# Kernel tuning notes

Measured on AMD Instinct MI355X. Metric: run time of the kernel, lower is better.

## Reference

```python
import jax, jax.numpy as jnp
import numpy as np

EPS = 1e-13

def masked_softmax(scores, mask):
    # scores: (B, L1, L2), mask: (B, L2) float {0,1}
    m = mask[:, None, :]
    # faithful to ESIM masked_softmax: softmax(scores * mask), re-mask, renormalize
    p = jax.nn.softmax(scores * m, axis=-1) * m
    return p / (jnp.sum(p, axis=-1, keepdims=True) + EPS)

def weighted_sum(values, weights, mask):
    # values: (B, Lv, H), weights: (B, Lq, Lv), mask: (B, Lq)
    out = jnp.einsum('bqv,bvh->bqh', weights, values)
    return out * mask[:, :, None]

def setup_inputs() -> dict:
    key = jax.random.key(0)
    k1, k2, k3, k4 = jax.random.split(key, 4)
    B, P, Q, H = 64, 1024, 1024, 256
    pre_batch = jax.random.normal(k1, (B, P, H), dtype=jnp.float32)
    hypo_batch = jax.random.normal(k2, (B, Q, H), dtype=jnp.float32)
    pre_mask = jax.random.randint(k3, (B, P), 0, 2, dtype=jnp.int32).at[:, 0].set(1)
    hypo_mask = jax.random.randint(k4, (B, Q), 0, 2, dtype=jnp.int32).at[:, 0].set(1)
    return {"pre_batch": pre_batch, "pre_mask": pre_mask,
            "hypo_batch": hypo_batch, "hypo_mask": hypo_mask}

def reference(pre_batch, pre_mask, hypo_batch, hypo_mask):
    pre_m = pre_mask.astype(pre_batch.dtype)
    hypo_m = hypo_mask.astype(hypo_batch.dtype)
    # similarity: (B, P, Q)
    similarity = jnp.einsum('bph,bqh->bpq', pre_batch, hypo_batch)
    pre_hypo_attn = masked_softmax(similarity, hypo_m)                       # (B,P,Q)
    hypo_pre_attn = masked_softmax(jnp.swapaxes(similarity, 1, 2), pre_m)    # (B,Q,P)
    attented_pre = weighted_sum(hypo_batch, pre_hypo_attn, pre_m)            # (B,P,H)
    attented_hypo = weighted_sum(pre_batch, hypo_pre_attn, hypo_m)           # (B,Q,H)
    return (attented_pre, attented_hypo)
```

## Files before the change

kernel.cpp:

```cpp
#include <hip/hip_runtime.h>
#include <stdint.h>

#define NB 64
#define NN 1024
#define NH 256

typedef _Float16 h8v __attribute__((ext_vector_type(8)));
typedef float    f4v __attribute__((ext_vector_type(4)));
typedef uint32_t u4v __attribute__((ext_vector_type(4)));
typedef uint32_t u2v __attribute__((ext_vector_type(2)));

static __device__ __forceinline__ uint32_t pack2h(float a, float b) {
  uint32_t ua = (uint32_t)__builtin_bit_cast(uint16_t, (_Float16)a);
  uint32_t ub = (uint32_t)__builtin_bit_cast(uint16_t, (_Float16)b);
  return ua | (ub << 16);
}

static __device__ __forceinline__ void gl_lds16(const void* g, void* l) {
  __builtin_amdgcn_global_load_lds(
      (const __attribute__((address_space(1))) uint32_t*)g,
      (__attribute__((address_space(3))) uint32_t*)l, 16, 0, 0);
}

__global__ __launch_bounds__(256)
void prep_tiles(const float* __restrict__ pre, const float* __restrict__ hypo,
                uint8_t* __restrict__ img)
{
  const int id = blockIdx.x;
  const int m  = id >> 11;
  const int bt = id & 2047;
  const float* src = (m ? hypo : pre) + (size_t)bt * (32 * NH);
  uint8_t* kimg = img + (size_t)id * 32768;
  uint8_t* vimg = kimg + 16384;

  __shared__ __align__(16) float ft[32 * 260];
  const int t = threadIdx.x, w = t >> 6, lane = t & 63;

#pragma unroll
  for (int i = 0; i < 8; ++i) {
    const int row = w * 8 + i;
    gl_lds16(src + row * NH + lane * 4, (uint8_t*)ft + row * 1040);
  }
  __syncthreads();

#pragma unroll
  for (int c = 0; c < 4; ++c) {
    const int k = c * 8 + (t >> 5);
    const uint32_t X = (uint32_t)((t & 31) * 16);
    const uint32_t h0 = ((X >> 4) ^ (uint32_t)(k & 7)) * 8;
    const uint8_t* p = (const uint8_t*)ft + k * 1040 + h0 * 4;
    f4v a0 = *(const f4v*)p;
    f4v a1 = *(const f4v*)(p + 16);
    u4v o; o[0] = pack2h(a0[0], a0[1]); o[1] = pack2h(a0[2], a0[3]);
    o[2] = pack2h(a1[0], a1[1]); o[3] = pack2h(a1[2], a1[3]);
    *(u4v*)(kimg + c * 4096 + t * 16) = o;
  }
  {
    const int g2 = t >> 6;
#pragma unroll
    for (int c = 0; c < 4; ++c) {
      const int h = c * 64 + (t & 63);
      float v[8];
#pragma unroll
      for (int j = 0; j < 4; ++j) v[j]     = ft[(4 * g2 + j) * 260 + h];
#pragma unroll
      for (int j = 0; j < 4; ++j) v[4 + j] = ft[(16 + 4 * g2 + j) * 260 + h];
      u4v o; o[0] = pack2h(v[0], v[1]); o[1] = pack2h(v[2], v[3]);
      o[2] = pack2h(v[4], v[5]); o[3] = pack2h(v[6], v[7]);
      *(u4v*)(vimg + g2 * 4096 + h * 16) = o;
    }
  }
}

__global__ __launch_bounds__(256, 2)
void attn_img(const uint8_t* __restrict__ img,
              const int* __restrict__ pre_mask, const int* __restrict__ hypo_mask,
              float* __restrict__ out)
{
  const int fid  = blockIdx.x;
  const int xcd  = fid & 7;
  const int s    = fid >> 3;
  const int bp   = xcd * 16 + (s >> 3);
  const int rblk = s & 7;
  const int pass = bp >> 6;
  const int b    = bp & 63;

  const uint8_t* qimg  = img + (size_t)(pass ? 1 : 0) * 67108864;
  const uint8_t* kvimg = img + (size_t)(pass ? 0 : 1) * 67108864;
  const int* kmask = pass == 0 ? hypo_mask : pre_mask;
  const int* qmask = pass == 0 ? pre_mask  : hypo_mask;
  float* outp = out + ((size_t)pass * NB + b) * NN * NH;
  const uint8_t* kvb = kvimg + (size_t)b * (32 * 32768);
  const int* kmb = kmask + b * NN;

  __shared__ __align__(16) uint8_t sbuf[2][32768];
  __shared__ __align__(16) float sbias[NN];

  const int t    = threadIdx.x;
  const int lane = t & 63;
  const int w    = t >> 6;
  const int g    = lane >> 4;
  const int q    = lane & 15;

  for (int i = t; i < NN; i += 256) sbias[i] = kmb[i] ? 0.f : -1e30f;

  h8v qf0[8], qf1[8];
  {
    const uint8_t* qb = qimg + (size_t)b * (32 * 32768);
#pragma unroll
    for (int ff = 0; ff < 2; ++ff) {
      const int qrow = rblk * 128 + w * 32 + ff * 16 + q;
      const uint8_t* qt = qb + (size_t)(qrow >> 5) * 32768 + (qrow & 31) * 512;
      const uint32_t swq = (uint32_t)((qrow & 7) << 4);
#pragma unroll
      for (int c = 0; c < 8; ++c) {
        h8v v = *(const h8v*)(qt + (((uint32_t)((c * 4 + g) << 4)) ^ swq));
        if (ff == 0) qf0[c] = v; else qf1[c] = v;
      }
    }
  }

  f4v accA[16], accB[16];
#pragma unroll
  for (int cf = 0; cf < 16; ++cf) { accA[cf] = (f4v){0,0,0,0}; accB[cf] = (f4v){0,0,0,0}; }
  float mrunA = -1e30f, lrunA = 0.f, mrunB = -1e30f, lrunB = 0.f;

#pragma unroll
  for (int i = 0; i < 8; ++i)
    gl_lds16(kvb + w * 8192 + i * 1024 + lane * 16, &sbuf[0][0] + w * 8192 + i * 1024);
  __syncthreads();

#pragma unroll 1
  for (int kt = 0; kt < 32; ++kt) {
    const int cur = kt & 1;
    if (kt < 31) {
      const uint8_t* kvt = kvb + (size_t)(kt + 1) * 32768;
#pragma unroll
      for (int i = 0; i < 8; ++i)
        gl_lds16(kvt + w * 8192 + i * 1024 + lane * 16,
                 &sbuf[cur ^ 1][0] + w * 8192 + i * 1024);
    }
    const uint8_t* sK = &sbuf[cur][0];
    const uint8_t* sV = sK + 16384;
    const int kb = kt * 32;

    const f4v b0 = *(const f4v*)&sbias[kb + 4 * g];
    const f4v b1 = *(const f4v*)&sbias[kb + 16 + 4 * g];

    f4v s0A = (f4v){0,0,0,0}, s1A = (f4v){0,0,0,0};
    f4v s0B = (f4v){0,0,0,0}, s1B = (f4v){0,0,0,0};
    __builtin_amdgcn_s_setprio(1);
#pragma unroll
    for (int c = 0; c < 8; ++c) {
      const uint32_t a0 = (uint32_t)(q * 512) + (((uint32_t)(c * 64 + g * 16)) ^ ((uint32_t)((q & 7) << 4)));
      h8v k0 = *(const h8v*)(sK + a0);
      h8v k1 = *(const h8v*)(sK + a0 + 8192);
      s0A = __builtin_amdgcn_mfma_f32_16x16x32_f16(k0, qf0[c], s0A, 0, 0, 0);
      s0B = __builtin_amdgcn_mfma_f32_16x16x32_f16(k0, qf1[c], s0B, 0, 0, 0);
      s1A = __builtin_amdgcn_mfma_f32_16x16x32_f16(k1, qf0[c], s1A, 0, 0, 0);
      s1B = __builtin_amdgcn_mfma_f32_16x16x32_f16(k1, qf1[c], s1B, 0, 0, 0);
    }
    __builtin_amdgcn_s_setprio(0);

    f4v sb0A, sb1A, sb0B, sb1B;
#pragma unroll
    for (int r = 0; r < 4; ++r) {
      sb0A[r] = s0A[r] + b0[r];  sb1A[r] = s1A[r] + b1[r];
      sb0B[r] = s0B[r] + b0[r];  sb1B[r] = s1B[r] + b1[r];
    }
    float tA = fmaxf(sb0A[0], sb1A[0]), tB = fmaxf(sb0B[0], sb1B[0]);
#pragma unroll
    for (int r = 1; r < 4; ++r) {
      tA = fmaxf(tA, fmaxf(sb0A[r], sb1A[r]));
      tB = fmaxf(tB, fmaxf(sb0B[r], sb1B[r]));
    }
    tA = fmaxf(tA, __shfl_xor(tA, 16));  tB = fmaxf(tB, __shfl_xor(tB, 16));
    tA = fmaxf(tA, __shfl_xor(tA, 32));  tB = fmaxf(tB, __shfl_xor(tB, 32));

    const bool grow = __any(fmaxf(tA - mrunA, tB - mrunB) > 8.0f);
    if (grow) {
      const float mnA = fmaxf(mrunA, tA), mnB = fmaxf(mrunB, tB);
      const float sA = __expf(mrunA - mnA), sB = __expf(mrunB - mnB);
      mrunA = mnA; mrunB = mnB;
      lrunA *= sA; lrunB *= sB;
#pragma unroll
      for (int cf = 0; cf < 16; ++cf) {
#pragma unroll
        for (int r = 0; r < 4; ++r) {
          accA[cf][r] *= sA;
          accB[cf][r] *= sB;
        }
      }
    }

    float pA[8], pB[8];
    float psA = 0.f, psB = 0.f;
#pragma unroll
    for (int r = 0; r < 4; ++r) {
      float a0 = __expf(sb0A[r] - mrunA);
      float a1 = __expf(sb1A[r] - mrunA);
      float b0e = __expf(sb0B[r] - mrunB);
      float b1e = __expf(sb1B[r] - mrunB);
      pA[r] = a0; pA[4 + r] = a1; psA += a0 + a1;
      pB[r] = b0e; pB[4 + r] = b1e; psB += b0e + b1e;
    }
    psA += __shfl_xor(psA, 16);  psB += __shfl_xor(psB, 16);
    psA += __shfl_xor(psA, 32);  psB += __shfl_xor(psB, 32);
    lrunA += psA; lrunB += psB;

    u4v au, bu;
    au[0] = pack2h(pA[0], pA[1]); au[1] = pack2h(pA[2], pA[3]);
    au[2] = pack2h(pA[4], pA[5]); au[3] = pack2h(pA[6], pA[7]);
    bu[0] = pack2h(pB[0], pB[1]); bu[1] = pack2h(pB[2], pB[3]);
    bu[2] = pack2h(pB[4], pB[5]); bu[3] = pack2h(pB[6], pB[7]);
    const h8v apA = __builtin_bit_cast(h8v, au);
    const h8v apB = __builtin_bit_cast(h8v, bu);

    __builtin_amdgcn_s_setprio(1);
#pragma unroll
    for (int cf = 0; cf < 16; ++cf) {
      h8v av = *(const h8v*)(sV + (uint32_t)(g * 4096 + (cf * 16 + q) * 16));
      accA[cf] = __builtin_amdgcn_mfma_f32_16x16x32_f16(av, apA, accA[cf], 0, 0, 0);
      accB[cf] = __builtin_amdgcn_mfma_f32_16x16x32_f16(av, apB, accB[cf], 0, 0, 0);
    }
    __builtin_amdgcn_s_setprio(0);

    __syncthreads();
  }

#pragma unroll
  for (int ff = 0; ff < 2; ++ff) {
    const float lrun = ff ? lrunB : lrunA;
    const int qrow = rblk * 128 + w * 32 + ff * 16 + q;
    const float fac = (float)qmask[b * NN + qrow] / lrun;
    float* op = outp + (size_t)qrow * NH;
#pragma unroll
    for (int cf = 0; cf < 16; ++cf) {
      f4v v = ff ? accB[cf] : accA[cf];
      v[0] *= fac; v[1] *= fac; v[2] *= fac; v[3] *= fac;
      *(f4v*)(op + cf * 16 + 4 * g) = v;
    }
  }
}

__global__ __launch_bounds__(256, 2)
void fused_dual_attn_fb(const float* __restrict__ pre,  const int* __restrict__ pre_mask,
                        const float* __restrict__ hypo, const int* __restrict__ hypo_mask,
                        float* __restrict__ out)
{
  const int pass = blockIdx.z;
  const float* Qm  = pass == 0 ? pre  : hypo;
  const float* KVm = pass == 0 ? hypo : pre;
  const int* kmask = pass == 0 ? hypo_mask : pre_mask;
  const int* qmask = pass == 0 ? pre_mask  : hypo_mask;
  float* outp = out + (size_t)pass * NB * NN * NH;

  const int b  = blockIdx.y;
  const int r0 = blockIdx.x * 64;

  __shared__ __align__(16) unsigned char sK [32 * NH * 2];
  __shared__ __align__(16) unsigned char sVt[NH * 16 * 4];
  __shared__ int smask[NN];

  const int t    = threadIdx.x;
  const int lane = t & 63;
  const int w    = t >> 6;
  const int g    = lane >> 4;
  const int q    = lane & 15;

  for (int i = t; i < NN; i += 256) smask[i] = kmask[b * NN + i];

  const int qrow = r0 + w * 16 + q;
  h8v qf[8];
  {
    const float* qp = Qm + ((size_t)b * NN + qrow) * NH + g * 8;
#pragma unroll
    for (int c = 0; c < 8; ++c) {
      f4v a0 = *(const f4v*)(qp + c * 32);
      f4v a1 = *(const f4v*)(qp + c * 32 + 4);
      h8v v;
      v[0] = (_Float16)a0[0]; v[1] = (_Float16)a0[1];
      v[2] = (_Float16)a0[2]; v[3] = (_Float16)a0[3];
      v[4] = (_Float16)a1[0]; v[5] = (_Float16)a1[1];
      v[6] = (_Float16)a1[2]; v[7] = (_Float16)a1[3];
      qf[c] = v;
    }
  }

  f4v acc[16];
#pragma unroll
  for (int cf = 0; cf < 16; ++cf) acc[cf] = (f4v){0.f, 0.f, 0.f, 0.f};
  float mrun = -1e30f, lrun = 0.f;

  const int skey = t & 31;
  const int m16  = (t >> 1) & 15;
  const int scb  = (t >> 5) << 2;
  const int odd  = skey & 1;

  for (int kb = 0; kb < NN; kb += 32) {
    __syncthreads();
#pragma unroll
    for (int i = 0; i < 8; ++i) {
      const int col = scb + 32 * i;
      f4v v = *(const f4v*)(KVm + ((size_t)b * NN + kb + skey) * NH + col);
      u2v d; d[0] = pack2h(v[0], v[1]); d[1] = pack2h(v[2], v[3]);
      uint32_t ka = (uint32_t)(skey * 512 + col * 2) ^ (uint32_t)((skey & 7) << 4);
      *(u2v*)(sK + ka) = d;
      float e = odd ? v[0] : v[2];
      float f = odd ? v[1] : v[3];
      float oe = __shfl_xor(e, 1);
      float of = __shfl_xor(f, 1);
      float lo0 = odd ? oe   : v[0];
      float hi0 = odd ? v[2] : oe;
      float lo1 = odd ? of   : v[1];
      float hi1 = odd ? v[3] : of;
      const int h0 = col + odd * 2;
      *(uint32_t*)(sVt + (uint32_t)((h0    ) * 64 + m16 * 4)) = pack2h(lo0, hi0);
      *(uint32_t*)(sVt + (uint32_t)((h0 + 1) * 64 + m16 * 4)) = pack2h(lo1, hi1);
    }
    __syncthreads();

    f4v s0 = (f4v){0.f,0.f,0.f,0.f}, s1 = (f4v){0.f,0.f,0.f,0.f};
#pragma unroll
    for (int c = 0; c < 8; ++c) {
      uint32_t a0 = ((uint32_t)(q * 512 + c * 64 + g * 16)) ^ (uint32_t)((q & 7) << 4);
      uint32_t a1 = ((uint32_t)((16 + q) * 512 + c * 64 + g * 16)) ^ (uint32_t)((q & 7) << 4);
      h8v k0 = *(const h8v*)(sK + a0);
      h8v k1 = *(const h8v*)(sK + a1);
      s0 = __builtin_amdgcn_mfma_f32_16x16x32_f16(k0, qf[c], s0, 0, 0, 0);
      s1 = __builtin_amdgcn_mfma_f32_16x16x32_f16(k1, qf[c], s1, 0, 0, 0);
    }

    int msk[8];
#pragma unroll
    for (int r = 0; r < 4; ++r) {
      msk[r]     = smask[kb + 4 * g + r];
      msk[4 + r] = smask[kb + 16 + 4 * g + r];
    }
    float tmax = -1e30f;
#pragma unroll
    for (int r = 0; r < 4; ++r)
      tmax = fmaxf(tmax, fmaxf(msk[r] ? s0[r] : -1e30f, msk[4 + r] ? s1[r] : -1e30f));
    tmax = fmaxf(tmax, __shfl_xor(tmax, 16));
    tmax = fmaxf(tmax, __shfl_xor(tmax, 32));
    const float mnew = fmaxf(mrun, tmax);
    const float scl = __expf(mrun - mnew);
    mrun = mnew;

    float p[8];
    float psum = 0.f;
#pragma unroll
    for (int r = 0; r < 4; ++r) {
      float p0 = msk[r]     ? __expf(s0[r] - mnew) : 0.f;
      float p1 = msk[4 + r] ? __expf(s1[r] - mnew) : 0.f;
      p[r] = p0; p[4 + r] = p1;
      psum += p0 + p1;
    }
    psum += __shfl_xor(psum, 16);
    psum += __shfl_xor(psum, 32);
    lrun = lrun * scl + psum;

    float srow[4];
#pragma unroll
    for (int r = 0; r < 4; ++r) srow[r] = __shfl(scl, 4 * g + r);
#pragma unroll
    for (int cf = 0; cf < 16; ++cf) {
#pragma unroll
      for (int r = 0; r < 4; ++r) acc[cf][r] *= srow[r];
    }

    uint32_t pf00 = pack2h(p[0], p[1]);
    uint32_t pf01 = pack2h(p[2], p[3]);
    uint32_t pf10 = pack2h(p[4], p[5]);
    uint32_t pf11 = pack2h(p[6], p[7]);
    const int srcA = q + 16 * ((2 * g) & 3);
    const int srcB = srcA + 16;
    uint32_t w0a = __shfl(pf00, srcA), w1a = __shfl(pf01, srcA);
    uint32_t w0b = __shfl(pf00, srcB), w1b = __shfl(pf01, srcB);
    uint32_t x0a = __shfl(pf10, srcA), x1a = __shfl(pf11, srcA);
    uint32_t x0b = __shfl(pf10, srcB), x1b = __shfl(pf11, srcB);
    u4v au;
    au[0] = (g >= 2) ? x0a : w0a;
    au[1] = (g >= 2) ? x1a : w1a;
    au[2] = (g >= 2) ? x0b : w0b;
    au[3] = (g >= 2) ? x1b : w1b;
    const h8v ap = __builtin_bit_cast(h8v, au);

#pragma unroll
    for (int cf = 0; cf < 16; ++cf) {
      h8v bv = *(const h8v*)(sVt + (uint32_t)((cf * 16 + q) * 64 + g * 16));
      acc[cf] = __builtin_amdgcn_mfma_f32_16x16x32_f16(ap, bv, acc[cf], 0, 0, 0);
    }
  }

  float fac[4];
#pragma unroll
  for (int r = 0; r < 4; ++r) {
    const float lr = __shfl(lrun, 4 * g + r);
    const int row = r0 + w * 16 + 4 * g + r;
    fac[r] = (float)qmask[b * NN + row] / lr;
  }
  float* op = outp + ((size_t)b * NN + r0 + w * 16) * NH;
#pragma unroll
  for (int cf = 0; cf < 16; ++cf) {
#pragma unroll
    for (int r = 0; r < 4; ++r) {
      op[(4 * g + r) * NH + cf * 16 + q] = acc[cf][r] * fac[r];
    }
  }
}

extern "C" void kernel_launch(void* const* d_in, const int* in_sizes, int n_in,
                              void* d_out, int out_size, void* d_ws, size_t ws_size,
                              hipStream_t stream) {
  const float* pre       = (const float*)d_in[0];
  const int*   pre_mask  = (const int*)d_in[1];
  const float* hypo      = (const float*)d_in[2];
  const int*   hypo_mask = (const int*)d_in[3];
  float* out = (float*)d_out;
  (void)in_sizes; (void)n_in; (void)out_size;

  if (ws_size >= (size_t)2 * 67108864) {
    uint8_t* img = (uint8_t*)d_ws;
    prep_tiles<<<dim3(4096), dim3(256), 0, stream>>>(pre, hypo, img);
    attn_img<<<dim3(1024), dim3(256), 0, stream>>>(img, pre_mask, hypo_mask, out);
  } else {
    fused_dual_attn_fb<<<dim3(16, 64, 2), dim3(256), 0, stream>>>(pre, pre_mask, hypo, hypo_mask, out);
  }
}
```

Measured before the change: 222.2 us.

## Halve query rows per block, single-buffer KV tile, raise occupancy to three blocks

Each wave now handles 16 query rows instead of 32, so each block covers 64 rows and the grid doubles to 2048 blocks. The KV shared buffer drops from double to single buffering, with a sync before and after each tile load. Launch bounds now ask for three blocks per CU. The goal is to cut registers and LDS per block so more waves are resident and hide latency. In exchange each K/V tile is reused by half as many query rows, which doubles total KV traffic, and the loss of prefetch exposes load latency unless other resident blocks cover it.

```diff
diff --git a/kernel.cpp b/kernel.cpp
--- a/kernel.cpp
+++ b/kernel.cpp
@@ -72,7 +72,7 @@
   }
 }
 
-__global__ __launch_bounds__(256, 2)
+__global__ __launch_bounds__(256, 3)
 void attn_img(const uint8_t* __restrict__ img,
               const int* __restrict__ pre_mask, const int* __restrict__ hypo_mask,
               float* __restrict__ out)
@@ -80,8 +80,8 @@
   const int fid  = blockIdx.x;
   const int xcd  = fid & 7;
   const int s    = fid >> 3;
-  const int bp   = xcd * 16 + (s >> 3);
-  const int rblk = s & 7;
+  const int bp   = xcd * 16 + (s >> 4);
+  const int rblk = s & 15;
   const int pass = bp >> 6;
   const int b    = bp & 63;
 
@@ -93,7 +93,7 @@
   const uint8_t* kvb = kvimg + (size_t)b * (32 * 32768);
   const int* kmb = kmask + b * NN;
 
-  __shared__ __align__(16) uint8_t sbuf[2][32768];
+  __shared__ __align__(16) uint8_t sbuf[32768];
   __shared__ __align__(16) float sbias[NN];
 
   const int t    = threadIdx.x;
@@ -104,139 +104,108 @@
 
   for (int i = t; i < NN; i += 256) sbias[i] = kmb[i] ? 0.f : -1e30f;
 
-  h8v qf0[8], qf1[8];
+  h8v qf[8];
   {
     const uint8_t* qb = qimg + (size_t)b * (32 * 32768);
-#pragma unroll
-    for (int ff = 0; ff < 2; ++ff) {
-      const int qrow = rblk * 128 + w * 32 + ff * 16 + q;
-      const uint8_t* qt = qb + (size_t)(qrow >> 5) * 32768 + (qrow & 31) * 512;
-      const uint32_t swq = (uint32_t)((qrow & 7) << 4);
-#pragma unroll
-      for (int c = 0; c < 8; ++c) {
-        h8v v = *(const h8v*)(qt + (((uint32_t)((c * 4 + g) << 4)) ^ swq));
-        if (ff == 0) qf0[c] = v; else qf1[c] = v;
-      }
-    }
-  }
-
-  f4v accA[16], accB[16];
-#pragma unroll
-  for (int cf = 0; cf < 16; ++cf) { accA[cf] = (f4v){0,0,0,0}; accB[cf] = (f4v){0,0,0,0}; }
-  float mrunA = -1e30f, lrunA = 0.f, mrunB = -1e30f, lrunB = 0.f;
-
-#pragma unroll
-  for (int i = 0; i < 8; ++i)
-    gl_lds16(kvb + w * 8192 + i * 1024 + lane * 16, &sbuf[0][0] + w * 8192 + i * 1024);
-  __syncthreads();
+    const int qrow = rblk * 64 + w * 16 + q;
+    const uint8_t* qt = qb + (size_t)(qrow >> 5) * 32768 + (qrow & 31) * 512;
+    const uint32_t swq = (uint32_t)((qrow & 7) << 4);
+#pragma unroll
+    for (int c = 0; c < 8; ++c)
+      qf[c] = *(const h8v*)(qt + (((uint32_t)((c * 4 + g) << 4)) ^ swq));
+  }
+
+  f4v acc[16];
+#pragma unroll
+  for (int cf = 0; cf < 16; ++cf) acc[cf] = (f4v){0, 0, 0, 0};
+  float mrun = -1e30f, lrun = 0.f;
 
 #pragma unroll 1
   for (int kt = 0; kt < 32; ++kt) {
-    const int cur = kt & 1;
-    if (kt < 31) {
-      const uint8_t* kvt = kvb + (size_t)(kt + 1) * 32768;
+    __syncthreads();
+    {
+      const uint8_t* ktile = kvb + (size_t)kt * 32768;
 #pragma unroll
       for (int i = 0; i < 8; ++i)
-        gl_lds16(kvt + w * 8192 + i * 1024 + lane * 16,
-                 &sbuf[cur ^ 1][0] + w * 8192 + i * 1024);
-    }
-    const uint8_t* sK = &sbuf[cur][0];
+        gl_lds16(ktile + w * 8192 + i * 1024 + lane * 16,
+                 &sbuf[0] + w * 8192 + i * 1024);
+    }
+    __syncthreads();
+
+    const uint8_t* sK = &sbuf[0];
     const uint8_t* sV = sK + 16384;
     const int kb = kt * 32;
 
     const f4v b0 = *(const f4v*)&sbias[kb + 4 * g];
     const f4v b1 = *(const f4v*)&sbias[kb + 16 + 4 * g];
 
-    f4v s0A = (f4v){0,0,0,0}, s1A = (f4v){0,0,0,0};
-    f4v s0B = (f4v){0,0,0,0}, s1B = (f4v){0,0,0,0};
+    f4v s0 = (f4v){0, 0, 0, 0}, s1 = (f4v){0, 0, 0, 0};
     __builtin_amdgcn_s_setprio(1);
 #pragma unroll
     for (int c = 0; c < 8; ++c) {
       const uint32_t a0 = (uint32_t)(q * 512) + (((uint32_t)(c * 64 + g * 16)) ^ ((uint32_t)((q & 7) << 4)));
       h8v k0 = *(const h8v*)(sK + a0);
       h8v k1 = *(const h8v*)(sK + a0 + 8192);
-      s0A = __builtin_amdgcn_mfma_f32_16x16x32_f16(k0, qf0[c], s0A, 0, 0, 0);
-      s0B = __builtin_amdgcn_mfma_f32_16x16x32_f16(k0, qf1[c], s0B, 0, 0, 0);
-      s1A = __builtin_amdgcn_mfma_f32_16x16x32_f16(k1, qf0[c], s1A, 0, 0, 0);
-      s1B = __builtin_amdgcn_mfma_f32_16x16x32_f16(k1, qf1[c], s1B, 0, 0, 0);
+      s0 = __builtin_amdgcn_mfma_f32_16x16x32_f16(k0, qf[c], s0, 0, 0, 0);
+      s1 = __builtin_amdgcn_mfma_f32_16x16x32_f16(k1, qf[c], s1, 0, 0, 0);
     }
     __builtin_amdgcn_s_setprio(0);
 
-    f4v sb0A, sb1A, sb0B, sb1B;
+    f4v sb0, sb1;
+#pragma unroll
+    for (int r = 0; r < 4; ++r) { sb0[r] = s0[r] + b0[r]; sb1[r] = s1[r] + b1[r]; }
+    float tmax = fmaxf(sb0[0], sb1[0]);
+#pragma unroll
+    for (int r = 1; r < 4; ++r) tmax = fmaxf(tmax, fmaxf(sb0[r], sb1[r]));
+    tmax = fmaxf(tmax, __shfl_xor(tmax, 16));
+    tmax = fmaxf(tmax, __shfl_xor(tmax, 32));
+
+    const bool grow = __any(tmax - mrun > 8.0f);
+    if (grow) {
+      const float mn = fmaxf(mrun, tmax);
+      const float sc = __expf(mrun - mn);
+      mrun = mn; lrun *= sc;
+#pragma unroll
+      for (int cf = 0; cf < 16; ++cf) {
+#pragma unroll
+        for (int r = 0; r < 4; ++r) acc[cf][r] *= sc;
+      }
+    }
+
+    float p[8];
+    float psum = 0.f;
 #pragma unroll
     for (int r = 0; r < 4; ++r) {
-      sb0A[r] = s0A[r] + b0[r];  sb1A[r] = s1A[r] + b1[r];
-      sb0B[r] = s0B[r] + b0[r];  sb1B[r] = s1B[r] + b1[r];
-    }
-    float tA = fmaxf(sb0A[0], sb1A[0]), tB = fmaxf(sb0B[0], sb1B[0]);
-#pragma unroll
-    for (int r = 1; r < 4; ++r) {
-      tA = fmaxf(tA, fmaxf(sb0A[r], sb1A[r]));
-      tB = fmaxf(tB, fmaxf(sb0B[r], sb1B[r]));
-    }
-    tA = fmaxf(tA, __shfl_xor(tA, 16));  tB = fmaxf(tB, __shfl_xor(tB, 16));
-    tA = fmaxf(tA, __shfl_xor(tA, 32));  tB = fmaxf(tB, __shfl_xor(tB, 32));
-
-    const bool grow = __any(fmaxf(tA - mrunA, tB - mrunB) > 8.0f);
-    if (grow) {
-      const float mnA = fmaxf(mrunA, tA), mnB = fmaxf(mrunB, tB);
-      const float sA = __expf(mrunA - mnA), sB = __expf(mrunB - mnB);
-      mrunA = mnA; mrunB = mnB;
-      lrunA *= sA; lrunB *= sB;
-#pragma unroll
-      for (int cf = 0; cf < 16; ++cf) {
-#pragma unroll
-        for (int r = 0; r < 4; ++r) {
-          accA[cf][r] *= sA;
-          accB[cf][r] *= sB;
-        }
-      }
-    }
-
-    float pA[8], pB[8];
-    float psA = 0.f, psB = 0.f;
-#pragma unroll
-    for (int r = 0; r < 4; ++r) {
-      float a0 = __expf(sb0A[r] - mrunA);
-      float a1 = __expf(sb1A[r] - mrunA);
-      float b0e = __expf(sb0B[r] - mrunB);
-      float b1e = __expf(sb1B[r] - mrunB);
-      pA[r] = a0; pA[4 + r] = a1; psA += a0 + a1;
-      pB[r] = b0e; pB[4 + r] = b1e; psB += b0e + b1e;
-    }
-    psA += __shfl_xor(psA, 16);  psB += __shfl_xor(psB, 16);
-    psA += __shfl_xor(psA, 32);  psB += __shfl_xor(psB, 32);
-    lrunA += psA; lrunB += psB;
-
-    u4v au, bu;
-    au[0] = pack2h(pA[0], pA[1]); au[1] = pack2h(pA[2], pA[3]);
-    au[2] = pack2h(pA[4], pA[5]); au[3] = pack2h(pA[6], pA[7]);
-    bu[0] = pack2h(pB[0], pB[1]); bu[1] = pack2h(pB[2], pB[3]);
-    bu[2] = pack2h(pB[4], pB[5]); bu[3] = pack2h(pB[6], pB[7]);
-    const h8v apA = __builtin_bit_cast(h8v, au);
-    const h8v apB = __builtin_bit_cast(h8v, bu);
+      float p0 = __expf(sb0[r] - mrun);
+      float p1 = __expf(sb1[r] - mrun);
+      p[r] = p0; p[4 + r] = p1;
+      psum += p0 + p1;
+    }
+    psum += __shfl_xor(psum, 16);
+    psum += __shfl_xor(psum, 32);
+    lrun += psum;
+
+    u4v au;
+    au[0] = pack2h(p[0], p[1]); au[1] = pack2h(p[2], p[3]);
+    au[2] = pack2h(p[4], p[5]); au[3] = pack2h(p[6], p[7]);
+    const h8v ap = __builtin_bit_cast(h8v, au);
 
     __builtin_amdgcn_s_setprio(1);
 #pragma unroll
     for (int cf = 0; cf < 16; ++cf) {
       h8v av = *(const h8v*)(sV + (uint32_t)(g * 4096 + (cf * 16 + q) * 16));
-      accA[cf] = __builtin_amdgcn_mfma_f32_16x16x32_f16(av, apA, accA[cf], 0, 0, 0);
-      accB[cf] = __builtin_amdgcn_mfma_f32_16x16x32_f16(av, apB, accB[cf], 0, 0, 0);
+      acc[cf] = __builtin_amdgcn_mfma_f32_16x16x32_f16(av, ap, acc[cf], 0, 0, 0);
     }
     __builtin_amdgcn_s_setprio(0);
-
-    __syncthreads();
-  }
-
-#pragma unroll
-  for (int ff = 0; ff < 2; ++ff) {
-    const float lrun = ff ? lrunB : lrunA;
-    const int qrow = rblk * 128 + w * 32 + ff * 16 + q;
+  }
+
+  {
+    const int qrow = rblk * 64 + w * 16 + q;
     const float fac = (float)qmask[b * NN + qrow] / lrun;
     float* op = outp + (size_t)qrow * NH;
 #pragma unroll
     for (int cf = 0; cf < 16; ++cf) {
-      f4v v = ff ? accB[cf] : accA[cf];
+      f4v v = acc[cf];
       v[0] *= fac; v[1] *= fac; v[2] *= fac; v[3] *= fac;
       *(f4v*)(op + cf * 16 + 4 * g) = v;
     }
@@ -423,7 +392,7 @@
   if (ws_size >= (size_t)2 * 67108864) {
     uint8_t* img = (uint8_t*)d_ws;
     prep_tiles<<<dim3(4096), dim3(256), 0, stream>>>(pre, hypo, img);
-    attn_img<<<dim3(1024), dim3(256), 0, stream>>>(img, pre_mask, hypo_mask, out);
+    attn_img<<<dim3(2048), dim3(256), 0, stream>>>(img, pre_mask, hypo_mask, out);
   } else {
     fused_dual_attn_fb<<<dim3(16, 64, 2), dim3(256), 0, stream>>>(pre, pre_mask, hypo, hypo_mask, out);
   }
```

Result: slower. 256.5 us (+15.4%).
